# Kernel tuning notes

Measured on AMD Instinct MI355X. Metric: run time of the kernel, lower is better.

Reference implementation:

```python
import jax, jax.numpy as jnp
import numpy as np

H = 1024
B, S = 8, 2048


def setup_inputs() -> dict:
    key = jax.random.key(0)
    ks = jax.random.split(key, 9)
    scale = 1.0 / np.sqrt(H)
    x = jax.random.normal(ks[0], (B, S, H), dtype=jnp.float32)
    attention_mask = jnp.ones((B, S), dtype=jnp.int32)
    wq = jax.random.uniform(ks[1], (H, H), jnp.float32, -scale, scale)
    bq = jax.random.uniform(ks[2], (H,), jnp.float32, -scale, scale)
    wk = jax.random.uniform(ks[3], (H, H), jnp.float32, -scale, scale)
    bk = jax.random.uniform(ks[4], (H,), jnp.float32, -scale, scale)
    wv = jax.random.uniform(ks[5], (H, H), jnp.float32, -scale, scale)
    bv = jax.random.uniform(ks[6], (H,), jnp.float32, -scale, scale)
    wo = jax.random.uniform(ks[7], (H, H), jnp.float32, -scale, scale)
    bo = jax.random.uniform(ks[8], (H,), jnp.float32, -scale, scale)
    return {"x": x, "attention_mask": attention_mask,
            "wq": wq, "bq": bq, "wk": wk, "bk": bk,
            "wv": wv, "bv": bv, "wo": wo, "bo": bo}


def reference(x, attention_mask, wq, bq, wk, bk, wv, bv, wo, bo):
    # x: [B, S, H]; attention_mask: [B, S] (1 = keep key, 0 = pad)
    hidden_dim = x.shape[-1]
    seq = x.shape[1]
    Q = jnp.einsum('bsh,dh->bsd', x, wq) + bq
    K = jnp.einsum('bsh,dh->bsd', x, wk) + bk
    V = jnp.einsum('bsh,dh->bsd', x, wv) + bv
    # scores: [B, S, S], scaled by 1/sqrt(hidden_dim) as in the original
    scores = jnp.einsum('bqd,bkd->bqk', Q, K) / jnp.sqrt(
        jnp.asarray(hidden_dim, dtype=x.dtype))
    causal = jnp.triu(jnp.ones((seq, seq), dtype=bool), k=1)  # [S, S]
    pad = ~(attention_mask.astype(bool))[:, None, :]          # [B, 1, S]
    mask = causal[None, :, :] | pad                           # [B, S, S]
    scores = jnp.where(mask, -jnp.inf, scores)
    probs = jax.nn.softmax(scores, axis=-1)
    # dropout_rate = 0.0 -> identity
    out = jnp.einsum('bqk,bkd->bqd', probs, V)
    out = jnp.einsum('bsd,hd->bsh', out, wo) + bo
    return out
```

## Files before the change

kernel.cpp:

```cpp
#include <hip/hip_runtime.h>
#include <hip/hip_bf16.h>


typedef __bf16 bf16x8 __attribute__((ext_vector_type(8)));
typedef float f32x4 __attribute__((ext_vector_type(4)));

static constexpr int HD = 1024;
static constexpr int BB = 8;
static constexpr int SS = 2048;
static constexpr long long SH = (long long)SS * HD;

__device__ __forceinline__ unsigned short f2bf(float f) {
  unsigned u = __builtin_bit_cast(unsigned, f);
  return (unsigned short)((u + 0x7FFFu + ((u >> 16) & 1u)) >> 16);
}
__device__ __forceinline__ f32x4 mfma16(bf16x8 a, bf16x8 b, f32x4 c) {
  return __builtin_amdgcn_mfma_f32_16x16x32_bf16(a, b, c, 0, 0, 0);
}
__device__ __forceinline__ void gload_lds16(const void* g, void* l) {
  __builtin_amdgcn_global_load_lds(
      (const __attribute__((address_space(1))) void*)g,
      (__attribute__((address_space(3))) void*)l, 16, 0, 0);
}

#define WAIT_LGKM0() do { asm volatile("s_waitcnt lgkmcnt(0)" ::: "memory"); \
  __builtin_amdgcn_sched_barrier(0); } while (0)
#define WAIT_VM(n) do { asm volatile("s_waitcnt vmcnt(" #n ")" ::: "memory"); \
  __builtin_amdgcn_sched_barrier(0); } while (0)

__device__ __forceinline__ bf16x8 read_frag(const unsigned short* tile, int row,
                                            int colb) {
  int byte = row * 128 + colb;
  byte ^= (row & 7) << 4;
  return *reinterpret_cast<const bf16x8*>(
      reinterpret_cast<const char*>(tile) + byte);
}

__device__ __forceinline__ void stage_half(const unsigned short* pM,
                                           long long ld, long long kt,
                                           unsigned short* tile, int h,
                                           int wid) {
  const unsigned short* s = pM + (long long)(h * 128) * ld + kt;
  gload_lds16(s, tile + h * 8192 + wid * 512);
  gload_lds16(s + 64 * ld, tile + h * 8192 + 4096 + wid * 512);
}

template <int MT, int Q>
__device__ __forceinline__ void ds_a(const unsigned short* At, int rA, int cb,
                                     bf16x8 af[2][2]) {
  constexpr int FPP = MT / 4;
#pragma unroll
  for (int f = 0; f < FPP; ++f) {
    af[f][0] = read_frag(At, rA + (FPP * Q + f) * 16, cb);
    af[f][1] = read_frag(At, rA + (FPP * Q + f) * 16, 64 + cb);
  }
}
__device__ __forceinline__ void ds_b(const unsigned short* Bt, int rB, int cb,
                                     bf16x8 B[4][2]) {
#pragma unroll
  for (int ni = 0; ni < 4; ++ni) {
    B[ni][0] = read_frag(Bt, rB + ni * 16, cb);
    B[ni][1] = read_frag(Bt, rB + ni * 16, 64 + cb);
  }
}
template <int MT, int Q>
__device__ __forceinline__ void mfma_q(const bf16x8 af[2][2],
                                       const bf16x8 B[4][2],
                                       f32x4 (&acc)[MT][4]) {
  constexpr int FPP = MT / 4;
#pragma unroll
  for (int f = 0; f < FPP; ++f)
#pragma unroll
    for (int ni = 0; ni < 4; ++ni) {
      acc[FPP * Q + f][ni] = mfma16(af[f][0], B[ni][0], acc[FPP * Q + f][ni]);
      acc[FPP * Q + f][ni] = mfma16(af[f][1], B[ni][1], acc[FPP * Q + f][ni]);
    }
}

#define PH_TAIL(QN, BRG) do { \
  __builtin_amdgcn_s_barrier(); \
  WAIT_LGKM0(); \
  __builtin_amdgcn_s_setprio(1); \
  mfma_q<MT, QN>(af, BRG, acc); \
  __builtin_amdgcn_s_setprio(0); \
  __builtin_amdgcn_s_barrier(); \
} while (0)

template <int MT>
__device__ __forceinline__ void run_tile(
    const unsigned short* pA, const unsigned short* pB, long long lda,
    long long ldb, int NT, unsigned short* As0, unsigned short* As1,
    unsigned short* Bs0, unsigned short* Bs1, int wid, int rA, int rB, int cb,
    f32x4 (&acc)[MT][4]) {
  bf16x8 BA[4][2], BB[4][2], af[2][2];
  stage_half(pA, lda, 0, As0, 0, wid);
  if constexpr (MT == 8) stage_half(pA, lda, 0, As0, 1, wid);
  stage_half(pB, ldb, 0, Bs0, 0, wid);
  stage_half(pB, ldb, 0, Bs0, 1, wid);
  stage_half(pB, ldb, 64, Bs1, 0, wid);
  stage_half(pB, ldb, 64, Bs1, 1, wid);
  WAIT_VM(4);
  __builtin_amdgcn_s_barrier();
  ds_b(Bs0, rB, cb, BA);
  WAIT_LGKM0();
  __builtin_amdgcn_s_barrier();

  const int NITER = NT / 2 - 1;
  for (int i = 0; i < NITER; ++i) {
    const long long kA1 = (long long)(2 * i + 1) * 64;
    const long long kN2 = (long long)(2 * i + 2) * 64;
    const long long kB3 = (long long)(2 * i + 3) * 64;
    ds_a<MT, 0>(As0, rA, cb, af); stage_half(pA, lda, kA1, As1, 0, wid); PH_TAIL(0, BA);
    ds_a<MT, 1>(As0, rA, cb, af);
    if constexpr (MT == 8) stage_half(pA, lda, kA1, As1, 1, wid);
    PH_TAIL(1, BA);
    ds_a<MT, 2>(As0, rA, cb, af); stage_half(pB, ldb, kN2, Bs0, 0, wid); PH_TAIL(2, BA);
    WAIT_VM(2);
    ds_a<MT, 3>(As0, rA, cb, af); ds_b(Bs1, rB, cb, BB);
    stage_half(pB, ldb, kN2, Bs0, 1, wid); PH_TAIL(3, BA);
    ds_a<MT, 0>(As1, rA, cb, af); stage_half(pA, lda, kN2, As0, 0, wid); PH_TAIL(0, BB);
    ds_a<MT, 1>(As1, rA, cb, af);
    if constexpr (MT == 8) stage_half(pA, lda, kN2, As0, 1, wid);
    PH_TAIL(1, BB);
    ds_a<MT, 2>(As1, rA, cb, af); stage_half(pB, ldb, kB3, Bs1, 0, wid); PH_TAIL(2, BB);
    WAIT_VM(2);
    ds_a<MT, 3>(As1, rA, cb, af); ds_b(Bs0, rB, cb, BA);
    stage_half(pB, ldb, kB3, Bs1, 1, wid); PH_TAIL(3, BB);
  }
  const long long kL = (long long)(NT - 1) * 64;
  ds_a<MT, 0>(As0, rA, cb, af); stage_half(pA, lda, kL, As1, 0, wid); PH_TAIL(0, BA);
  ds_a<MT, 1>(As0, rA, cb, af);
  if constexpr (MT == 8) stage_half(pA, lda, kL, As1, 1, wid);
  PH_TAIL(1, BA);
  ds_a<MT, 2>(As0, rA, cb, af); PH_TAIL(2, BA);
  WAIT_VM(0);
  ds_a<MT, 3>(As0, rA, cb, af); ds_b(Bs1, rB, cb, BB); PH_TAIL(3, BA);
  ds_a<MT, 0>(As1, rA, cb, af); PH_TAIL(0, BB);
  ds_a<MT, 1>(As1, rA, cb, af); PH_TAIL(1, BB);
  ds_a<MT, 2>(As1, rA, cb, af); PH_TAIL(2, BB);
  ds_a<MT, 3>(As1, rA, cb, af); PH_TAIL(3, BB);
}

struct TC {
  int wid, lane, wm, wn, rA, rB, cb, rr, ccl, rowt, colg;
};
template <int MT>
__device__ __forceinline__ TC tc_setup() {
  TC t;
  const int tid = threadIdx.x;
  t.wid = tid >> 6;
  t.lane = tid & 63;
  t.wm = t.wid >> 2;
  t.wn = t.wid & 3;
  const int l16 = t.lane & 15;
  t.rA = t.wm * (MT * 16) + l16;
  t.rB = t.wn * 64 + l16;
  t.cb = (t.lane >> 4) * 16;
  t.rr = (t.lane >> 4) * 4;
  t.ccl = l16;
  t.rowt = tid >> 3;
  t.colg = (((tid & 7) ^ ((tid >> 3) & 7)) * 8);
  return t;
}

#define SHARED_TILES8() \
  __shared__ __align__(16) unsigned short As0[16384], As1[16384]; \
  __shared__ __align__(16) unsigned short Bs0[16384], Bs1[16384]
#define SHARED_TILES4() \
  __shared__ __align__(16) unsigned short As0[8192], As1[8192]; \
  __shared__ __align__(16) unsigned short Bs0[16384], Bs1[16384]

__global__ __launch_bounds__(512, 2) void qk_kernel(
    const unsigned short* __restrict__ X, const unsigned short* __restrict__ W,
    const float* __restrict__ bq, const float* __restrict__ bk,
    unsigned short* __restrict__ Q, unsigned short* __restrict__ K) {
  SHARED_TILES8();
  const int lin = blockIdx.y * 8 + blockIdx.x;
  const int swz = (lin & 7) * 64 + (lin >> 3);
  const int m0 = (swz >> 3) * 256, n0 = (swz & 7) * 256;
  TC t = tc_setup<8>();
  const unsigned short* pA = X + (long long)(m0 + t.rowt) * HD + t.colg;
  const unsigned short* pB = W + (long long)(n0 + t.rowt) * HD + t.colg;
  f32x4 acc[8][4] = {};
  run_tile<8>(pA, pB, HD, HD, 16, As0, As1, Bs0, Bs1, t.wid, t.rA, t.rB, t.cb, acc);
#pragma unroll
  for (int mi = 0; mi < 8; ++mi)
#pragma unroll
    for (int ni = 0; ni < 4; ++ni) {
      const int gn = n0 + t.wn * 64 + ni * 16 + t.ccl;
      const float bias = (gn < 1024) ? bq[gn] : bk[gn - 1024];
      unsigned short* dst = (gn < 1024) ? (Q + gn) : (K + gn - 1024);
#pragma unroll
      for (int j = 0; j < 4; ++j) {
        const int gm = m0 + t.wm * 128 + mi * 16 + t.rr + j;
        dst[(long long)gm * HD] = f2bf(acc[mi][ni][j] + bias);
      }
    }
}

__global__ __launch_bounds__(512, 2) void vt_kernel(
    const unsigned short* __restrict__ Wv, const unsigned short* __restrict__ X,
    const float* __restrict__ bv, unsigned short* __restrict__ Vt) {
  SHARED_TILES8();
  const int lin = blockIdx.x;
  const int swz = (lin & 7) * 32 + (lin >> 3);
  const int m0 = (swz & 3) * 256, n0 = (swz >> 2) * 256;
  TC t = tc_setup<8>();
  const unsigned short* pA = Wv + (long long)(m0 + t.rowt) * HD + t.colg;
  const unsigned short* pB = X + (long long)(n0 + t.rowt) * HD + t.colg;
  f32x4 acc[8][4] = {};
  run_tile<8>(pA, pB, HD, HD, 16, As0, As1, Bs0, Bs1, t.wid, t.rA, t.rB, t.cb, acc);
#pragma unroll
  for (int mi = 0; mi < 8; ++mi)
#pragma unroll
    for (int ni = 0; ni < 4; ++ni) {
      const int gn = n0 + t.wn * 64 + ni * 16 + t.ccl;
      const long long base = (long long)(gn >> 11) * SH + (gn & 2047);
#pragma unroll
      for (int j = 0; j < 4; ++j) {
        const int gm = m0 + t.wm * 128 + mi * 16 + t.rr + j;
        Vt[base + (long long)gm * SS] = f2bf(acc[mi][ni][j] + bv[gm]);
      }
    }
}

__global__ __launch_bounds__(512, 2) void scores_kernel(
    const unsigned short* __restrict__ Q, const unsigned short* __restrict__ Km,
    const int* __restrict__ mask, unsigned short* __restrict__ S,
    float* __restrict__ rowsum) {
  SHARED_TILES8();
  const int bid = blockIdx.x;
  const long long b = bid & 7;
  int tt = bid >> 3;
  int ii = 0, base = 0;
  while (tt >= base + ii + 1) { base += ii + 1; ++ii; }
  const int jj = tt - base;
  const int m0 = ii * 256, n0 = jj * 256;
  TC t = tc_setup<8>();
  const unsigned short* pA = Q + b * SH + (long long)(m0 + t.rowt) * HD + t.colg;
  const unsigned short* pB = Km + b * SH + (long long)(n0 + t.rowt) * HD + t.colg;
  f32x4 acc[8][4] = {};
  run_tile<8>(pA, pB, HD, HD, 16, As0, As1, Bs0, Bs1, t.wid, t.rA, t.rB, t.cb, acc);

  unsigned short* Sb = S + b * (long long)SS * SS;
  const int* mb = mask + b * SS;
  float* rs = rowsum + b * SS;
  float* rsl = reinterpret_cast<float*>(As0);
#pragma unroll
  for (int mi = 0; mi < 8; ++mi)
#pragma unroll
    for (int j = 0; j < 4; ++j) {
      const int gm = m0 + t.wm * 128 + mi * 16 + t.rr + j;
      float rsum = 0.0f;
#pragma unroll
      for (int ni = 0; ni < 4; ++ni) {
        const int gn = n0 + t.wn * 64 + ni * 16 + t.ccl;
        const bool dead = (gn > gm) || (mb[gn] == 0);
        const float pv = dead ? 0.0f : __expf(acc[mi][ni][j] * 0.03125f);
        Sb[(long long)gm * SS + gn] = f2bf(pv);
        rsum += pv;
      }
#pragma unroll
      for (int o = 1; o < 16; o <<= 1) rsum += __shfl_xor(rsum, o);
      if (t.ccl == 0) rsl[t.wn * 256 + (t.wm * 128 + mi * 16 + t.rr + j)] = rsum;
    }
  __syncthreads();
  const int tid = threadIdx.x;
  if (tid < 256) {
    const float v = rsl[tid] + rsl[256 + tid] + rsl[512 + tid] + rsl[768 + tid];
    atomicAdd(&rs[m0 + tid], v);
  }
}

__global__ __launch_bounds__(512, 2) void pv_kernel(
    const unsigned short* __restrict__ S, const unsigned short* __restrict__ Vt,
    const float* __restrict__ rowsum, unsigned short* __restrict__ AO) {
  SHARED_TILES4();
  const int bid = blockIdx.x;
  const long long b = bid & 7;
  const int r = bid >> 3;
  const int p = r & 7;
  const int n0 = (r >> 3) * 256;
  const unsigned short* Sb = S + b * (long long)SS * SS;
  const unsigned short* Vb = Vt + b * SH;
  const float* rs = rowsum + b * SS;
  TC t = tc_setup<4>();

  for (int pass = 0; pass < 2; ++pass) {
    const int mi0 = pass ? 15 - p : p;
    const int m0 = mi0 * 128;
    const int NT = 2 * (mi0 + 1);
    const unsigned short* pA = Sb + (long long)(m0 + t.rowt) * SS + t.colg;
    const unsigned short* pB = Vb + (long long)(n0 + t.rowt) * SS + t.colg;
    f32x4 acc[4][4] = {};
    run_tile<4>(pA, pB, SS, SS, NT, As0, As1, Bs0, Bs1, t.wid, t.rA, t.rB,
                t.cb, acc);
#pragma unroll
    for (int mi = 0; mi < 4; ++mi)
#pragma unroll
      for (int j = 0; j < 4; ++j) {
        const int gm = m0 + t.wm * 64 + mi * 16 + t.rr + j;
        const float inv = 1.0f / rs[gm];
#pragma unroll
        for (int ni = 0; ni < 4; ++ni) {
          const int gn = n0 + t.wn * 64 + ni * 16 + t.ccl;
          AO[(b * SS + gm) * (long long)HD + gn] = f2bf(acc[mi][ni][j] * inv);
        }
      }
  }
}

__global__ __launch_bounds__(512, 2) void oproj_kernel(
    const unsigned short* __restrict__ AO, const unsigned short* __restrict__ W,
    const float* __restrict__ bo, float* __restrict__ out) {
  SHARED_TILES8();
  const int lin = blockIdx.x;
  const int swz = (lin & 7) * 32 + (lin >> 3);
  const int n0 = (swz & 3) * 256, m0 = (swz >> 2) * 256;
  TC t = tc_setup<8>();
  const unsigned short* pA = AO + (long long)(m0 + t.rowt) * HD + t.colg;
  const unsigned short* pB = W + (long long)(n0 + t.rowt) * HD + t.colg;
  f32x4 acc[8][4] = {};
  run_tile<8>(pA, pB, HD, HD, 16, As0, As1, Bs0, Bs1, t.wid, t.rA, t.rB, t.cb, acc);
#pragma unroll
  for (int mi = 0; mi < 8; ++mi)
#pragma unroll
    for (int ni = 0; ni < 4; ++ni) {
      const int gn = n0 + t.wn * 64 + ni * 16 + t.ccl;
      const float bias = bo[gn];
#pragma unroll
      for (int j = 0; j < 4; ++j) {
        const int gm = m0 + t.wm * 128 + mi * 16 + t.rr + j;
        out[(long long)gm * HD + gn] = acc[mi][ni][j] + bias;
      }
    }
}

__global__ __launch_bounds__(256) void cast_all(
    const float* __restrict__ x, const float* __restrict__ wq,
    const float* __restrict__ wk, const float* __restrict__ wv,
    const float* __restrict__ wo, unsigned short* __restrict__ xb,
    unsigned short* __restrict__ wqkb, unsigned short* __restrict__ wvb,
    unsigned short* __restrict__ wob, float* __restrict__ rowsum) {
  const int NX4 = (int)((long long)BB * SS * HD / 4);
  const int W4 = HD * HD / 4;
  const int RS4 = BB * SS / 4;
  const int TOT = NX4 + 4 * W4 + RS4;
  int idx = blockIdx.x * blockDim.x + threadIdx.x;
  const int stride = gridDim.x * blockDim.x;
  for (int u = idx; u < TOT; u += stride) {
    if (u >= NX4 + 4 * W4) {
      *reinterpret_cast<float4*>(rowsum + (u - NX4 - 4 * W4) * 4) =
          make_float4(0.f, 0.f, 0.f, 0.f);
      continue;
    }
    const float* src;
    unsigned short* dst;
    int off;
    if (u < NX4) {
      src = x; dst = xb; off = u;
    } else {
      const int v = u - NX4;
      const int seg = v >> 18;
      off = v & (W4 - 1);
      if (seg == 0) { src = wq; dst = wqkb; }
      else if (seg == 1) { src = wk; dst = wqkb + HD * HD; }
      else if (seg == 2) { src = wv; dst = wvb; }
      else { src = wo; dst = wob; }
    }
    float4 f = *reinterpret_cast<const float4*>(src + off * 4);
    ushort4 o;
    o.x = f2bf(f.x); o.y = f2bf(f.y); o.z = f2bf(f.z); o.w = f2bf(f.w);
    *reinterpret_cast<ushort4*>(dst + off * 4) = o;
  }
}

extern "C" void kernel_launch(void* const* d_in, const int* in_sizes, int n_in,
                              void* d_out, int out_size, void* d_ws, size_t ws_size,
                              hipStream_t stream) {
  const float* x = (const float*)d_in[0];
  const int* amask = (const int*)d_in[1];
  const float* wq = (const float*)d_in[2];
  const float* bq = (const float*)d_in[3];
  const float* wk = (const float*)d_in[4];
  const float* bk = (const float*)d_in[5];
  const float* wv = (const float*)d_in[6];
  const float* bv = (const float*)d_in[7];
  const float* wo = (const float*)d_in[8];
  const float* bo = (const float*)d_in[9];
  float* out = (float*)d_out;

  const long long NX = (long long)BB * SS * HD;
  char* p = (char*)d_ws;
  unsigned short* xb = (unsigned short*)p;    p += NX * 2;
  unsigned short* wqkb = (unsigned short*)p;  p += 2LL * HD * HD * 2;
  unsigned short* wvb = (unsigned short*)p;   p += (long long)HD * HD * 2;
  unsigned short* wob = (unsigned short*)p;   p += (long long)HD * HD * 2;
  unsigned short* Qb = (unsigned short*)p;    p += NX * 2;
  unsigned short* Kb = (unsigned short*)p;    p += NX * 2;
  unsigned short* Vtb = (unsigned short*)p;   p += NX * 2;
  unsigned short* Sb = (unsigned short*)p;    p += (long long)BB * SS * SS * 2;
  float* rowsum = (float*)p;                  p += (long long)BB * SS * 4;
  unsigned short* AOb = xb;

  cast_all<<<dim3(2048), 256, 0, stream>>>(x, wq, wk, wv, wo, xb, wqkb, wvb,
                                           wob, rowsum);

  qk_kernel<<<dim3(8, 64), 512, 0, stream>>>(xb, wqkb, bq, bk, Qb, Kb);
  vt_kernel<<<dim3(256), 512, 0, stream>>>(wvb, xb, bv, Vtb);

  scores_kernel<<<dim3(288), 512, 0, stream>>>(Qb, Kb, amask, Sb, rowsum);
  pv_kernel<<<dim3(256), 512, 0, stream>>>(Sb, Vtb, rowsum, AOb);

  oproj_kernel<<<dim3(256), 512, 0, stream>>>(AOb, wob, bo, out);
}
```

Measured before the change: 330.0 us.

## Merge V projection and scores kernels into one launch; relax vmcnt waits

Combines the V-transpose projection and the causal scores/exp kernel into a single 544-block launch. Independent work now shares one grid, which fills the GPU better (256+288 blocks) and removes one launch and its tail. The GEMM main loop's vmcnt waits are also reworked to allow more outstanding global-to-LDS loads per phase. That adds prefetch depth but risks a race if the counts are wrong.

After: 327.3 us. Within noise of the previous version (-0.8%).

```diff
diff --git a/kernel.cpp b/kernel.cpp
--- a/kernel.cpp
+++ b/kernel.cpp
@@ -110,6 +110,7 @@
     const long long kA1 = (long long)(2 * i + 1) * 64;
     const long long kN2 = (long long)(2 * i + 2) * 64;
     const long long kB3 = (long long)(2 * i + 3) * 64;
+    WAIT_VM(4);
     ds_a<MT, 0>(As0, rA, cb, af); stage_half(pA, lda, kA1, As1, 0, wid); PH_TAIL(0, BA);
     ds_a<MT, 1>(As0, rA, cb, af);
     if constexpr (MT == 8) stage_half(pA, lda, kA1, As1, 1, wid);
@@ -123,18 +124,20 @@
     if constexpr (MT == 8) stage_half(pA, lda, kN2, As0, 1, wid);
     PH_TAIL(1, BB);
     ds_a<MT, 2>(As1, rA, cb, af); stage_half(pB, ldb, kB3, Bs1, 0, wid); PH_TAIL(2, BB);
-    WAIT_VM(2);
+    if constexpr (MT == 8) WAIT_VM(6); else WAIT_VM(4);
     ds_a<MT, 3>(As1, rA, cb, af); ds_b(Bs0, rB, cb, BA);
     stage_half(pB, ldb, kB3, Bs1, 1, wid); PH_TAIL(3, BB);
   }
   const long long kL = (long long)(NT - 1) * 64;
+  WAIT_VM(4);
   ds_a<MT, 0>(As0, rA, cb, af); stage_half(pA, lda, kL, As1, 0, wid); PH_TAIL(0, BA);
   ds_a<MT, 1>(As0, rA, cb, af);
   if constexpr (MT == 8) stage_half(pA, lda, kL, As1, 1, wid);
   PH_TAIL(1, BA);
   ds_a<MT, 2>(As0, rA, cb, af); PH_TAIL(2, BA);
+  if constexpr (MT == 8) WAIT_VM(4); else WAIT_VM(2);
+  ds_a<MT, 3>(As0, rA, cb, af); ds_b(Bs1, rB, cb, BB); PH_TAIL(3, BA);
   WAIT_VM(0);
-  ds_a<MT, 3>(As0, rA, cb, af); ds_b(Bs1, rB, cb, BB); PH_TAIL(3, BA);
   ds_a<MT, 0>(As1, rA, cb, af); PH_TAIL(0, BB);
   ds_a<MT, 1>(As1, rA, cb, af); PH_TAIL(1, BB);
   ds_a<MT, 2>(As1, rA, cb, af); PH_TAIL(2, BB);
@@ -198,77 +201,80 @@
     }
 }
 
-__global__ __launch_bounds__(512, 2) void vt_kernel(
+__global__ __launch_bounds__(512, 2) void mid_kernel(
     const unsigned short* __restrict__ Wv, const unsigned short* __restrict__ X,
-    const float* __restrict__ bv, unsigned short* __restrict__ Vt) {
-  SHARED_TILES8();
-  const int lin = blockIdx.x;
-  const int swz = (lin & 7) * 32 + (lin >> 3);
-  const int m0 = (swz & 3) * 256, n0 = (swz >> 2) * 256;
-  TC t = tc_setup<8>();
-  const unsigned short* pA = Wv + (long long)(m0 + t.rowt) * HD + t.colg;
-  const unsigned short* pB = X + (long long)(n0 + t.rowt) * HD + t.colg;
-  f32x4 acc[8][4] = {};
-  run_tile<8>(pA, pB, HD, HD, 16, As0, As1, Bs0, Bs1, t.wid, t.rA, t.rB, t.cb, acc);
-#pragma unroll
-  for (int mi = 0; mi < 8; ++mi)
-#pragma unroll
-    for (int ni = 0; ni < 4; ++ni) {
-      const int gn = n0 + t.wn * 64 + ni * 16 + t.ccl;
-      const long long base = (long long)(gn >> 11) * SH + (gn & 2047);
-#pragma unroll
-      for (int j = 0; j < 4; ++j) {
-        const int gm = m0 + t.wm * 128 + mi * 16 + t.rr + j;
-        Vt[base + (long long)gm * SS] = f2bf(acc[mi][ni][j] + bv[gm]);
-      }
-    }
-}
-
-__global__ __launch_bounds__(512, 2) void scores_kernel(
+    const float* __restrict__ bv, unsigned short* __restrict__ Vt,
     const unsigned short* __restrict__ Q, const unsigned short* __restrict__ Km,
     const int* __restrict__ mask, unsigned short* __restrict__ S,
     float* __restrict__ rowsum) {
   SHARED_TILES8();
-  const int bid = blockIdx.x;
-  const long long b = bid & 7;
-  int tt = bid >> 3;
-  int ii = 0, base = 0;
-  while (tt >= base + ii + 1) { base += ii + 1; ++ii; }
-  const int jj = tt - base;
-  const int m0 = ii * 256, n0 = jj * 256;
   TC t = tc_setup<8>();
-  const unsigned short* pA = Q + b * SH + (long long)(m0 + t.rowt) * HD + t.colg;
-  const unsigned short* pB = Km + b * SH + (long long)(n0 + t.rowt) * HD + t.colg;
-  f32x4 acc[8][4] = {};
-  run_tile<8>(pA, pB, HD, HD, 16, As0, As1, Bs0, Bs1, t.wid, t.rA, t.rB, t.cb, acc);
-
-  unsigned short* Sb = S + b * (long long)SS * SS;
-  const int* mb = mask + b * SS;
-  float* rs = rowsum + b * SS;
-  float* rsl = reinterpret_cast<float*>(As0);
-#pragma unroll
-  for (int mi = 0; mi < 8; ++mi)
-#pragma unroll
-    for (int j = 0; j < 4; ++j) {
-      const int gm = m0 + t.wm * 128 + mi * 16 + t.rr + j;
-      float rsum = 0.0f;
+  if (blockIdx.x < 256) {
+    const int lin = blockIdx.x;
+    const int swz = (lin & 7) * 32 + (lin >> 3);
+    const int m0 = (swz & 3) * 256, n0 = (swz >> 2) * 256;
+    const unsigned short* pA = Wv + (long long)(m0 + t.rowt) * HD + t.colg;
+    const unsigned short* pB = X + (long long)(n0 + t.rowt) * HD + t.colg;
+    f32x4 acc[8][4] = {};
+    run_tile<8>(pA, pB, HD, HD, 16, As0, As1, Bs0, Bs1, t.wid, t.rA, t.rB,
+                t.cb, acc);
+#pragma unroll
+    for (int mi = 0; mi < 8; ++mi)
 #pragma unroll
       for (int ni = 0; ni < 4; ++ni) {
         const int gn = n0 + t.wn * 64 + ni * 16 + t.ccl;
-        const bool dead = (gn > gm) || (mb[gn] == 0);
-        const float pv = dead ? 0.0f : __expf(acc[mi][ni][j] * 0.03125f);
-        Sb[(long long)gm * SS + gn] = f2bf(pv);
-        rsum += pv;
+        const long long base = (long long)(gn >> 11) * SH + (gn & 2047);
+#pragma unroll
+        for (int j = 0; j < 4; ++j) {
+          const int gm = m0 + t.wm * 128 + mi * 16 + t.rr + j;
+          Vt[base + (long long)gm * SS] = f2bf(acc[mi][ni][j] + bv[gm]);
+        }
       }
-#pragma unroll
-      for (int o = 1; o < 16; o <<= 1) rsum += __shfl_xor(rsum, o);
-      if (t.ccl == 0) rsl[t.wn * 256 + (t.wm * 128 + mi * 16 + t.rr + j)] = rsum;
-    }
-  __syncthreads();
-  const int tid = threadIdx.x;
-  if (tid < 256) {
-    const float v = rsl[tid] + rsl[256 + tid] + rsl[512 + tid] + rsl[768 + tid];
-    atomicAdd(&rs[m0 + tid], v);
+  } else {
+    const int s = blockIdx.x - 256;
+    const long long b = s & 7;
+    int tt = s >> 3;
+    int ii = 0, base = 0;
+    while (tt >= base + ii + 1) { base += ii + 1; ++ii; }
+    const int jj = tt - base;
+    const int m0 = ii * 256, n0 = jj * 256;
+    const unsigned short* pA =
+        Q + b * SH + (long long)(m0 + t.rowt) * HD + t.colg;
+    const unsigned short* pB =
+        Km + b * SH + (long long)(n0 + t.rowt) * HD + t.colg;
+    f32x4 acc[8][4] = {};
+    run_tile<8>(pA, pB, HD, HD, 16, As0, As1, Bs0, Bs1, t.wid, t.rA, t.rB,
+                t.cb, acc);
+    unsigned short* Sb = S + b * (long long)SS * SS;
+    const int* mb = mask + b * SS;
+    float* rs = rowsum + b * SS;
+    float* rsl = reinterpret_cast<float*>(As0);
+#pragma unroll
+    for (int mi = 0; mi < 8; ++mi)
+#pragma unroll
+      for (int j = 0; j < 4; ++j) {
+        const int gm = m0 + t.wm * 128 + mi * 16 + t.rr + j;
+        float rsum = 0.0f;
+#pragma unroll
+        for (int ni = 0; ni < 4; ++ni) {
+          const int gn = n0 + t.wn * 64 + ni * 16 + t.ccl;
+          const bool dead = (gn > gm) || (mb[gn] == 0);
+          const float pv = dead ? 0.0f : __expf(acc[mi][ni][j] * 0.03125f);
+          Sb[(long long)gm * SS + gn] = f2bf(pv);
+          rsum += pv;
+        }
+#pragma unroll
+        for (int o = 1; o < 16; o <<= 1) rsum += __shfl_xor(rsum, o);
+        if (t.ccl == 0)
+          rsl[t.wn * 256 + (t.wm * 128 + mi * 16 + t.rr + j)] = rsum;
+      }
+    __syncthreads();
+    const int tid = threadIdx.x;
+    if (tid < 256) {
+      const float v =
+          rsl[tid] + rsl[256 + tid] + rsl[512 + tid] + rsl[768 + tid];
+      atomicAdd(&rs[m0 + tid], v);
+    }
   }
 }
 
@@ -407,9 +413,10 @@
                                            wob, rowsum);
 
   qk_kernel<<<dim3(8, 64), 512, 0, stream>>>(xb, wqkb, bq, bk, Qb, Kb);
-  vt_kernel<<<dim3(256), 512, 0, stream>>>(wvb, xb, bv, Vtb);
-
-  scores_kernel<<<dim3(288), 512, 0, stream>>>(Qb, Kb, amask, Sb, rowsum);
+
+  mid_kernel<<<dim3(544), 512, 0, stream>>>(wvb, xb, bv, Vtb, Qb, Kb, amask,
+                                            Sb, rowsum);
+
   pv_kernel<<<dim3(256), 512, 0, stream>>>(Sb, Vtb, rowsum, AOb);
 
   oproj_kernel<<<dim3(256), 512, 0, stream>>>(AOb, wob, bo, out);
```
